# Kernel tuning notes

Hardware: AMD Instinct MI355X
Metric: run time of the kernel (lower is better)

Reference implementation:

```python
import jax, jax.numpy as jnp
import numpy as np

L = 8          # n_layer
D = 512        # hidden_size
DIN = 1024     # d_inner = 2*D (Mamba expand=2)
DS = 16        # d_state
DTR = 32       # dt_rank = ceil(D/16)
K = 4          # d_conv
NACT = 3       # n_action_to_predict
ADIM = 4
LOSS_COEF = 1.0

def silu(x):
    return x * jax.nn.sigmoid(x)

def rms(x, w, eps=1e-5):
    return x * jax.lax.rsqrt(jnp.mean(x * x, axis=-1, keepdims=True) + eps) * w

def tokenize(images, states, actions, patch_w, patch_b, state_w, state_b, act_w, act_b):
    # images [b,l,3,224,224] -> 14x14 patches of 3*16*16=768 -> mean-pooled image token
    b, l = images.shape[:2]
    p = images.reshape(b, l, 3, 14, 16, 14, 16).transpose(0, 1, 3, 5, 2, 4, 6).reshape(b, l, 196, 768)
    img = jnp.mean(p @ patch_w.T + patch_b, axis=2)            # [b,l,D] token_type 1
    st = states[:, :, 0] @ state_w.T + state_b                 # [b,l,D] token_type 2
    ac = actions[:, :, :NACT - 1] @ act_w.T + act_b            # [b,l,NACT-1,D] token_type 3
    toks = jnp.concatenate([img[:, :, None], st[:, :, None], ac], axis=2)  # [b,l,1+NACT,D]
    return toks.reshape(b, l * (1 + NACT), D)

def mamba_mixer(x, in_w, cw, cb, xpw, dtw, dtb, alog, dp, ow):
    # x: [b,S,D]
    b, S, _ = x.shape
    xz = x @ in_w.T                                   # [b,S,2*DIN]
    xi, z = xz[..., :DIN], xz[..., DIN:]
    # causal depthwise conv, kernel K
    xp = jnp.pad(xi, ((0, 0), (K - 1, 0), (0, 0)))
    xc = cb + sum(cw[:, k] * xp[:, k:k + S, :] for k in range(K))
    xc = silu(xc)
    proj = xc @ xpw.T                                  # [b,S,DTR+2*DS]
    dtr, Bm, Cm = proj[..., :DTR], proj[..., DTR:DTR + DS], proj[..., DTR + DS:]
    dt = jax.nn.softplus(dtr @ dtw.T + dtb)            # [b,S,DIN]
    A = -jnp.exp(alog)                                 # [DIN,DS]
    dA = jnp.exp(dt[..., None] * A)                    # [b,S,DIN,DS]
    dBx = dt[..., None] * Bm[:, :, None, :] * xc[..., None]
    def step(h, inp):
        a_t, bx_t = inp
        h = a_t * h + bx_t
        return h, h
    _, hs = jax.lax.scan(step, jnp.zeros((b, DIN, DS), x.dtype),
                         (dA.swapaxes(0, 1), dBx.swapaxes(0, 1)))  # hs [S,b,DIN,DS]
    y = jnp.einsum('sbdn,bsn->bsd', hs, Cm) + dp * xc
    return (y * silu(z)) @ ow.T

def _forward(images, seq_length, states, actions, action_labels,
             patch_w, patch_b, state_w, state_b, act_w, act_b,
             norm1_w, in_proj_w, conv_w, conv_b, x_proj_w, dt_w, dt_b,
             A_log, Dp, out_proj_w, norm2_w, fc1_w, fc2_w, norm_f_w,
             head_w, head_b):
    b, l = images.shape[:2]
    hidden = tokenize(images, states, actions, patch_w, patch_b, state_w, state_b, act_w, act_b)
    residual = jnp.zeros_like(hidden)
    for i in range(L):
        residual = hidden + residual
        hidden = mamba_mixer(rms(residual, norm1_w[i]), in_proj_w[i], conv_w[i], conv_b[i],
                             x_proj_w[i], dt_w[i], dt_b[i], A_log[i], Dp[i], out_proj_w[i])
        residual = hidden + residual
        g = rms(residual, norm2_w[i]) @ fc1_w[i].T       # GatedMLP fc1 -> [.., 2*DIN]
        hidden = (g[..., :DIN] * silu(g[..., DIN:])) @ fc2_w[i].T
    residual = hidden + residual
    hidden = rms(residual, norm_f_w)
    # static action-token positions: per-frame tokens [img, state, act, act] -> indices 1..3
    hs = hidden.reshape(b, l, 1 + NACT, D)[:, :, 1:, :]
    action_preds = hs @ head_w.T + head_b                # [b,l,NACT,ADIM]
    mask = (jnp.arange(l)[None, :] < seq_length[:, None]).astype(jnp.float32)
    la = jnp.mean(jnp.abs(action_preds - action_labels), axis=(2, 3))
    la = (la * mask).sum(axis=1) / jnp.clip(mask.sum(axis=1), 1.0)
    loss = jnp.mean(la) * LOSS_COEF
    return loss, action_preds

def setup_inputs() -> dict:
    key = jax.random.key(0)
    ks = iter(jax.random.split(key, 40))
    nrm = lambda shape, s=0.02: s * jax.random.normal(next(ks), shape, dtype=jnp.float32)
    inp = {
        'images': jax.random.normal(next(ks), (2, 64, 3, 224, 224), jnp.float32),
        'seq_length': jax.random.randint(next(ks), (2,), 1, 65),
        'states': jax.random.normal(next(ks), (2, 64, NACT, 7), jnp.float32),
        'actions': jax.random.normal(next(ks), (2, 64, NACT, ADIM), jnp.float32),
        'action_labels': jax.random.normal(next(ks), (2, 64, NACT, ADIM), jnp.float32),
        'patch_w': nrm((D, 768)), 'patch_b': jnp.zeros((D,), jnp.float32),
        'state_w': nrm((D, 7)), 'state_b': jnp.zeros((D,), jnp.float32),
        'act_w': nrm((D, ADIM)), 'act_b': jnp.zeros((D,), jnp.float32),
        'norm1_w': jnp.ones((L, D), jnp.float32),
        'in_proj_w': nrm((L, 2 * DIN, D)),
        'conv_w': nrm((L, DIN, K), 0.1), 'conv_b': jnp.zeros((L, DIN), jnp.float32),
        'x_proj_w': nrm((L, DTR + 2 * DS, DIN)),
        'dt_w': nrm((L, DIN, DTR)), 'dt_b': jnp.full((L, DIN), -4.6, jnp.float32),
        'A_log': jnp.log(jnp.broadcast_to(jnp.arange(1, DS + 1, dtype=jnp.float32), (L, DIN, DS))).copy(),
        'Dp': jnp.ones((L, DIN), jnp.float32),
        'out_proj_w': nrm((L, D, DIN)),
        'norm2_w': jnp.ones((L, D), jnp.float32),
        'fc1_w': nrm((L, 2 * DIN, D)), 'fc2_w': nrm((L, D, DIN)),
        'norm_f_w': jnp.ones((D,), jnp.float32),
        'head_w': nrm((ADIM, D)), 'head_b': jnp.zeros((ADIM,), jnp.float32),
    }
    return inp

def reference(images, seq_length, states, actions, action_labels,
              patch_w, patch_b, state_w, state_b, act_w, act_b,
              norm1_w, in_proj_w, conv_w, conv_b, x_proj_w, dt_w, dt_b,
              A_log, Dp, out_proj_w, norm2_w, fc1_w, fc2_w, norm_f_w,
              head_w, head_b):
    return _forward(images, seq_length, states, actions, action_labels,
                    patch_w, patch_b, state_w, state_b, act_w, act_b,
                    norm1_w, in_proj_w, conv_w, conv_b, x_proj_w, dt_w, dt_b,
                    A_log, Dp, out_proj_w, norm2_w, fc1_w, fc2_w, norm_f_w,
                    head_w, head_b)
```

## Files before the change

### kernel.cpp

```cpp
#include <hip/hip_runtime.h>


#define NTOK 512
#define SEQ  256
#define CS   32
#define NC   8

typedef __attribute__((ext_vector_type(8))) short bf16x8;
typedef __attribute__((ext_vector_type(16))) float f32x16;

__device__ __forceinline__ float silu_f(float x) { return x / (1.0f + expf(-x)); }
__device__ __forceinline__ float softplus_f(float x) {
  return (x > 20.0f) ? x : log1pf(expf(x));
}

__device__ __forceinline__ void split_pack(float4 v, uint2* hi, uint2* lo) {
  uint ux = __float_as_uint(v.x), uy = __float_as_uint(v.y);
  uint uz = __float_as_uint(v.z), uw = __float_as_uint(v.w);
  hi->x = (ux >> 16) | (uy & 0xffff0000u);
  hi->y = (uz >> 16) | (uw & 0xffff0000u);
  float lx = v.x - __uint_as_float(ux & 0xffff0000u);
  float ly = v.y - __uint_as_float(uy & 0xffff0000u);
  float lz = v.z - __uint_as_float(uz & 0xffff0000u);
  float lw = v.w - __uint_as_float(uw & 0xffff0000u);
  lo->x = (__float_as_uint(lx) >> 16) | (__float_as_uint(ly) & 0xffff0000u);
  lo->y = (__float_as_uint(lz) >> 16) | (__float_as_uint(lw) & 0xffff0000u);
}

__global__ __launch_bounds__(256) void gemm_bs_k(const float* __restrict__ A,
                                                 const float* __restrict__ B,
                                                 float* __restrict__ C,
                                                 int M, int N, int K, int Kc) {
  __shared__ alignas(16) ushort sAh[2][2][512];
  __shared__ alignas(16) ushort sAl[2][2][512];
  __shared__ alignas(16) ushort sBh[2][2][512];
  __shared__ alignas(16) ushort sBl[2][2][512];
  int t = threadIdx.x;
  int bn = blockIdx.x, bm = blockIdx.y, z = blockIdx.z;
  const float* Ab = A + (size_t)bm * 64 * K + (size_t)z * Kc;
  const float* Bb = B + (size_t)bn * 64 * K + (size_t)z * Kc;
  float* Cb = C + (size_t)z * M * N;
  int r = t >> 2, kc = (t & 3) << 2;
  int st = r >> 5, m = r & 31;
  int off = ((kc >> 3) << 8) + (m << 3) + (kc & 7);
  int w = t >> 6, lane = t & 63;
  int wr = w >> 1, wc = w & 1;

  f32x16 acc;
#pragma unroll
  for (int i = 0; i < 16; ++i) acc[i] = 0.f;

  int nk = Kc >> 4;
  float4 a4 = *(const float4*)&Ab[(size_t)r * K + kc];
  float4 b4 = *(const float4*)&Bb[(size_t)r * K + kc];
  {
    uint2 hi, lo;
    split_pack(a4, &hi, &lo);
    *(uint2*)&sAh[0][st][off] = hi; *(uint2*)&sAl[0][st][off] = lo;
    split_pack(b4, &hi, &lo);
    *(uint2*)&sBh[0][st][off] = hi; *(uint2*)&sBl[0][st][off] = lo;
  }
  __syncthreads();
  for (int ks = 0; ks < nk; ++ks) {
    int buf = ks & 1;
    if (ks + 1 < nk) {
      a4 = *(const float4*)&Ab[(size_t)r * K + (ks + 1) * 16 + kc];
      b4 = *(const float4*)&Bb[(size_t)r * K + (ks + 1) * 16 + kc];
    }
    bf16x8 ah = *(bf16x8*)&sAh[buf][wr][lane << 3];
    bf16x8 al = *(bf16x8*)&sAl[buf][wr][lane << 3];
    bf16x8 bh = *(bf16x8*)&sBh[buf][wc][lane << 3];
    bf16x8 bl = *(bf16x8*)&sBl[buf][wc][lane << 3];
    acc = __builtin_amdgcn_mfma_f32_32x32x16_bf16(ah, bh, acc, 0, 0, 0);
    acc = __builtin_amdgcn_mfma_f32_32x32x16_bf16(al, bh, acc, 0, 0, 0);
    acc = __builtin_amdgcn_mfma_f32_32x32x16_bf16(ah, bl, acc, 0, 0, 0);
    if (ks + 1 < nk) {
      uint2 hi, lo;
      split_pack(a4, &hi, &lo);
      *(uint2*)&sAh[buf ^ 1][st][off] = hi; *(uint2*)&sAl[buf ^ 1][st][off] = lo;
      split_pack(b4, &hi, &lo);
      *(uint2*)&sBh[buf ^ 1][st][off] = hi; *(uint2*)&sBl[buf ^ 1][st][off] = lo;
    }
    __syncthreads();
  }
  int col = lane & 31, rq = lane >> 5;
  float* Cw = Cb + (size_t)(bm * 64 + wr * 32) * N + bn * 64 + wc * 32 + col;
#pragma unroll
  for (int rg = 0; rg < 16; ++rg) {
    int row = (rg & 3) + ((rg >> 2) << 3) + (rq << 2);
    Cw[(size_t)row * N] = acc[rg];
  }
}

__global__ __launch_bounds__(256) void gemm_glu_k(const float* __restrict__ G,
                                                  const float* __restrict__ B,
                                                  float* __restrict__ C,
                                                  int M, int N, int K, int Kc) {
  __shared__ alignas(16) ushort sAh[2][2][512];
  __shared__ alignas(16) ushort sAl[2][2][512];
  __shared__ alignas(16) ushort sBh[2][2][512];
  __shared__ alignas(16) ushort sBl[2][2][512];
  int t = threadIdx.x;
  int bn = blockIdx.x, bm = blockIdx.y, z = blockIdx.z;
  const float* Gb = G + (size_t)bm * 64 * 2048 + (size_t)z * Kc;
  const float* Bb = B + (size_t)bn * 64 * K + (size_t)z * Kc;
  float* Cb = C + (size_t)z * M * N;
  int r = t >> 2, kc = (t & 3) << 2;
  int st = r >> 5, m = r & 31;
  int off = ((kc >> 3) << 8) + (m << 3) + (kc & 7);
  int w = t >> 6, lane = t & 63;
  int wr = w >> 1, wc = w & 1;

  f32x16 acc;
#pragma unroll
  for (int i = 0; i < 16; ++i) acc[i] = 0.f;

  int nk = Kc >> 4;
  const float* gr = Gb + (size_t)r * 2048 + kc;
  float4 ga = *(const float4*)&gr[0];
  float4 gz = *(const float4*)&gr[1024];
  float4 b4 = *(const float4*)&Bb[(size_t)r * K + kc];
  {
    float4 a4 = {ga.x * silu_f(gz.x), ga.y * silu_f(gz.y),
                 ga.z * silu_f(gz.z), ga.w * silu_f(gz.w)};
    uint2 hi, lo;
    split_pack(a4, &hi, &lo);
    *(uint2*)&sAh[0][st][off] = hi; *(uint2*)&sAl[0][st][off] = lo;
    split_pack(b4, &hi, &lo);
    *(uint2*)&sBh[0][st][off] = hi; *(uint2*)&sBl[0][st][off] = lo;
  }
  __syncthreads();
  for (int ks = 0; ks < nk; ++ks) {
    int buf = ks & 1;
    if (ks + 1 < nk) {
      ga = *(const float4*)&gr[(ks + 1) * 16];
      gz = *(const float4*)&gr[1024 + (ks + 1) * 16];
      b4 = *(const float4*)&Bb[(size_t)r * K + (ks + 1) * 16 + kc];
    }
    bf16x8 ah = *(bf16x8*)&sAh[buf][wr][lane << 3];
    bf16x8 al = *(bf16x8*)&sAl[buf][wr][lane << 3];
    bf16x8 bh = *(bf16x8*)&sBh[buf][wc][lane << 3];
    bf16x8 bl = *(bf16x8*)&sBl[buf][wc][lane << 3];
    acc = __builtin_amdgcn_mfma_f32_32x32x16_bf16(ah, bh, acc, 0, 0, 0);
    acc = __builtin_amdgcn_mfma_f32_32x32x16_bf16(al, bh, acc, 0, 0, 0);
    acc = __builtin_amdgcn_mfma_f32_32x32x16_bf16(ah, bl, acc, 0, 0, 0);
    if (ks + 1 < nk) {
      float4 a4 = {ga.x * silu_f(gz.x), ga.y * silu_f(gz.y),
                   ga.z * silu_f(gz.z), ga.w * silu_f(gz.w)};
      uint2 hi, lo;
      split_pack(a4, &hi, &lo);
      *(uint2*)&sAh[buf ^ 1][st][off] = hi; *(uint2*)&sAl[buf ^ 1][st][off] = lo;
      split_pack(b4, &hi, &lo);
      *(uint2*)&sBh[buf ^ 1][st][off] = hi; *(uint2*)&sBl[buf ^ 1][st][off] = lo;
    }
    __syncthreads();
  }
  int col = lane & 31, rq = lane >> 5;
  float* Cw = Cb + (size_t)(bm * 64 + wr * 32) * N + bn * 64 + wc * 32 + col;
#pragma unroll
  for (int rg = 0; rg < 16; ++rg) {
    int row = (rg & 3) + ((rg >> 2) << 3) + (rq << 2);
    Cw[(size_t)row * N] = acc[rg];
  }
}

__global__ void patch_part_k(const float* __restrict__ img, float* __restrict__ pmp) {
  int blk = blockIdx.x;
  int bl = blk / 14, hb = blk % 14;
  int t = threadIdx.x;
  int c = t >> 6, hi = (t >> 2) & 15, wi4 = t & 3;
  const float* base = img + (size_t)bl * 3 * 50176 + (size_t)c * 50176 +
                      (size_t)(hb * 16 + hi) * 224 + wi4 * 4;
  float4 s = {0.f, 0.f, 0.f, 0.f};
#pragma unroll
  for (int wb = 0; wb < 14; ++wb) {
    float4 v = *(const float4*)&base[wb * 16];
    s.x += v.x; s.y += v.y; s.z += v.z; s.w += v.w;
  }
  ((float4*)(pmp + (size_t)blk * 768))[t] = s;
}

__global__ void patch_red_k(const float* __restrict__ pmp, float* __restrict__ meanp) {
  int bl = blockIdx.x;
  int t = threadIdx.x;
  float4 s = {0.f, 0.f, 0.f, 0.f};
  for (int hb = 0; hb < 14; ++hb) {
    float4 v = ((const float4*)(pmp + (size_t)(bl * 14 + hb) * 768))[t];
    s.x += v.x; s.y += v.y; s.z += v.z; s.w += v.w;
  }
  const float inv = 1.0f / 196.0f;
  float4 o = {s.x * inv, s.y * inv, s.z * inv, s.w * inv};
  ((float4*)(meanp + (size_t)bl * 768))[t] = o;
}

__global__ void tokenize_k(const float* __restrict__ imgp,
                           const float* __restrict__ states,
                           const float* __restrict__ actions,
                           const float* __restrict__ pb,
                           const float* __restrict__ sw, const float* __restrict__ sb,
                           const float* __restrict__ aw, const float* __restrict__ ab,
                           float* __restrict__ hidden, float* __restrict__ residual) {
  int tok = blockIdx.x;
  int t = threadIdx.x;
  int j = tok & 3;
  int bl = tok >> 2;
  int o0 = t * 4;
  float out[4];
  if (j == 0) {
    float4 a = ((const float4*)pb)[t];
    const float* ip = imgp + (size_t)bl * 512;
#pragma unroll
    for (int p = 0; p < 8; ++p) {
      float4 v = ((const float4*)(ip + (size_t)p * 65536))[t];
      a.x += v.x; a.y += v.y; a.z += v.z; a.w += v.w;
    }
    out[0] = a.x; out[1] = a.y; out[2] = a.z; out[3] = a.w;
  } else if (j == 1) {
    const float* sv = states + (size_t)bl * 21;
#pragma unroll
    for (int i = 0; i < 4; ++i) {
      int o = o0 + i;
      float acc = sb[o];
      for (int k = 0; k < 7; ++k) acc += sw[o * 7 + k] * sv[k];
      out[i] = acc;
    }
  } else {
    const float* av = actions + ((size_t)bl * 3 + (j - 2)) * 4;
#pragma unroll
    for (int i = 0; i < 4; ++i) {
      int o = o0 + i;
      float acc = ab[o];
      for (int k = 0; k < 4; ++k) acc += aw[o * 4 + k] * av[k];
      out[i] = acc;
    }
  }
  float4 ov = {out[0], out[1], out[2], out[3]};
  ((float4*)(hidden + (size_t)tok * 512))[t] = ov;
  float4 z4 = {0.f, 0.f, 0.f, 0.f};
  ((float4*)(residual + (size_t)tok * 512))[t] = z4;
}

__global__ void addnorm_k(const float* __restrict__ hid, int parts,
                          float* __restrict__ res,
                          const float* __restrict__ w, float* __restrict__ xn) {
  int tok = blockIdx.x;
  int t = threadIdx.x;
  float4* r4 = (float4*)(res + (size_t)tok * 512);
  float4 r = r4[t];
  const float4* hp = (const float4*)(hid + (size_t)tok * 512);
  for (int p = 0; p < parts; ++p) {
    float4 h = hp[t];
    r.x += h.x; r.y += h.y; r.z += h.z; r.w += h.w;
    hp += 65536;
  }
  r4[t] = r;
  float ss = r.x * r.x + r.y * r.y + r.z * r.z + r.w * r.w;
  for (int off = 32; off; off >>= 1) ss += __shfl_down(ss, off, 64);
  __shared__ float s2[2];
  if ((t & 63) == 0) s2[t >> 6] = ss;
  __syncthreads();
  float tot = s2[0] + s2[1];
  float scale = rsqrtf(tot * (1.0f / 512.0f) + 1e-5f);
  float4 wv = ((const float4*)w)[t];
  float4 o = {r.x * scale * wv.x, r.y * scale * wv.y,
              r.z * scale * wv.z, r.w * scale * wv.w};
  ((float4*)(xn + (size_t)tok * 512))[t] = o;
}

__global__ __launch_bounds__(256) void convproj_k(const float* __restrict__ xz,
                                                  const float* __restrict__ cw,
                                                  const float* __restrict__ cb,
                                                  const float* __restrict__ xpw,
                                                  const float* __restrict__ dtw,
                                                  const float* __restrict__ dtbias,
                                                  float* __restrict__ xc,
                                                  float* __restrict__ proj,
                                                  float* __restrict__ dt) {
  int tok = blockIdx.x;
  int t = threadIdx.x;
  int b = tok >> 8, s = tok & 255;
  __shared__ float xr[1024];
  __shared__ float pp[4][64];
  __shared__ float pr[64];
  int d4 = t * 4;
  float4 cw0 = ((const float4*)cw)[d4];
  float4 cw1 = ((const float4*)cw)[d4 + 1];
  float4 cw2 = ((const float4*)cw)[d4 + 2];
  float4 cw3 = ((const float4*)cw)[d4 + 3];
  float acc0 = cb[d4], acc1 = cb[d4 + 1], acc2 = cb[d4 + 2], acc3 = cb[d4 + 3];
  const float* base = xz + (size_t)b * 256 * 2048 + d4;
  const float wk0[4] = {cw0.x, cw0.y, cw0.z, cw0.w};
  const float wk1[4] = {cw1.x, cw1.y, cw1.z, cw1.w};
  const float wk2[4] = {cw2.x, cw2.y, cw2.z, cw2.w};
  const float wk3[4] = {cw3.x, cw3.y, cw3.z, cw3.w};
#pragma unroll
  for (int k = 0; k < 4; ++k) {
    int row = s + k - 3;
    if (row >= 0) {
      float4 v = *(const float4*)&base[(size_t)row * 2048];
      acc0 += wk0[k] * v.x; acc1 += wk1[k] * v.y;
      acc2 += wk2[k] * v.z; acc3 += wk3[k] * v.w;
    }
  }
  float4 xc4 = {silu_f(acc0), silu_f(acc1), silu_f(acc2), silu_f(acc3)};
  ((float4*)(xc + (size_t)tok * 1024))[t] = xc4;
  *(float4*)&xr[d4] = xc4;
  __syncthreads();
  int n = t & 63, q = t >> 6;
  {
    const float* wrow = xpw + (size_t)n * 1024 + q * 256;
    const float* xq = xr + q * 256;
    float acc = 0.f;
    for (int k = 0; k < 256; k += 4)
      acc += wrow[k] * xq[k] + wrow[k + 1] * xq[k + 1] +
             wrow[k + 2] * xq[k + 2] + wrow[k + 3] * xq[k + 3];
    pp[q][n] = acc;
  }
  __syncthreads();
  if (t < 64) {
    float v = pp[0][t] + pp[1][t] + pp[2][t] + pp[3][t];
    pr[t] = v;
    proj[(size_t)tok * 64 + t] = v;
  }
  __syncthreads();
#pragma unroll
  for (int i = 0; i < 4; ++i) {
    int d = t * 4 + i;
    const float* dw = dtw + (size_t)d * 32;
    float a = dtbias[d];
    for (int k = 0; k < 32; ++k) a += dw[k] * pr[k];
    dt[(size_t)tok * 1024 + d] = softplus_f(a);
  }
}

__global__ __launch_bounds__(128) void scan1_k(const float* __restrict__ dt,
                                               const float* __restrict__ proj,
                                               const float* __restrict__ xc,
                                               const float* __restrict__ alog,
                                               float2* __restrict__ pairs) {
  __shared__ float sDt[CS][8];
  __shared__ float sXc[CS][8];
  __shared__ float sB[CS][16];
  int t = threadIdx.x;
  int g = blockIdx.x, c = blockIdx.y;
  int b = g >> 7;
  int d0 = (g & 127) << 3;
  int dl = t >> 4, n = t & 15;
  int d = d0 + dl;
  int s0 = c * CS;
  float A = -expf(alog[d * 16 + n]);
  const float* dtb = dt + ((size_t)b * SEQ + s0) * 1024 + d0;
  const float* xcb = xc + ((size_t)b * SEQ + s0) * 1024 + d0;
  const float* pbp = proj + ((size_t)b * SEQ + s0) * 64 + 32;
  if (t < 64) {
    int li = t >> 1, lc4 = (t & 1) * 4;
    *(float4*)&sDt[li][lc4] = *(const float4*)&dtb[(size_t)li * 1024 + lc4];
    *(float4*)&sXc[li][lc4] = *(const float4*)&xcb[(size_t)li * 1024 + lc4];
  }
  {
    int r = t >> 2, c4 = (t & 3) * 4;
    *(float4*)&sB[r][c4] = *(const float4*)&pbp[(size_t)r * 64 + c4];
  }
  __syncthreads();
  float Ap = 1.f, Bacc = 0.f;
#pragma unroll
  for (int i = 0; i < CS; ++i) {
    float dtv = sDt[i][dl];
    float dA = __expf(dtv * A);
    Bacc = dA * Bacc + dtv * sB[i][n] * sXc[i][dl];
    Ap *= dA;
  }
  pairs[(((size_t)c * 2 + b) * 1024 + d) * 16 + n] = make_float2(Ap, Bacc);
}

__global__ __launch_bounds__(128) void scan2_k(const float* __restrict__ dt,
                                               const float* __restrict__ proj,
                                               const float* __restrict__ xc,
                                               const float* __restrict__ xz,
                                               const float* __restrict__ alog,
                                               const float* __restrict__ Dp,
                                               const float2* __restrict__ pairs,
                                               float* __restrict__ yz) {
  __shared__ float sDt[CS][8];
  __shared__ float sXc[CS][8];
  __shared__ float sZ[CS][8];
  __shared__ float sBC[CS][32];
  __shared__ float sY[CS][8];
  int t = threadIdx.x;
  int g = blockIdx.x, c = blockIdx.y;
  int b = g >> 7;
  int d0 = (g & 127) << 3;
  int dl = t >> 4, n = t & 15;
  int d = d0 + dl;
  int s0 = c * CS;
  float A = -expf(alog[d * 16 + n]);
  float dp = Dp[d];
  const float* dtb = dt + ((size_t)b * SEQ + s0) * 1024 + d0;
  const float* xcb = xc + ((size_t)b * SEQ + s0) * 1024 + d0;
  const float* zb  = xz + ((size_t)b * SEQ + s0) * 2048 + 1024 + d0;
  const float* pbp = proj + ((size_t)b * SEQ + s0) * 64 + 32;
  float* yb = yz + ((size_t)b * SEQ + s0) * 1024 + d0;
  float h = 0.f;
  for (int cc = 0; cc < c; ++cc) {
    float2 p = pairs[(((size_t)cc * 2 + b) * 1024 + d) * 16 + n];
    h = p.x * h + p.y;
  }
  bool lowh = t < 64;
  int u = lowh ? t : t - 64;
  int li = u >> 1, lc4 = (u & 1) * 4;
  if (lowh) {
    *(float4*)&sDt[li][lc4] = *(const float4*)&dtb[(size_t)li * 1024 + lc4];
    *(float4*)&sXc[li][lc4] = *(const float4*)&xcb[(size_t)li * 1024 + lc4];
  } else {
    *(float4*)&sZ[li][lc4] = *(const float4*)&zb[(size_t)li * 2048 + lc4];
  }
  {
    int v0i = t >> 3, v0c = (t & 7) * 4;
    int v1i = (t + 128) >> 3, v1c = ((t + 128) & 7) * 4;
    *(float4*)&sBC[v0i][v0c] = *(const float4*)&pbp[(size_t)v0i * 64 + v0c];
    *(float4*)&sBC[v1i][v1c] = *(const float4*)&pbp[(size_t)v1i * 64 + v1c];
  }
  __syncthreads();
#pragma unroll
  for (int i = 0; i < CS; ++i) {
    float dtv = sDt[i][dl];
    float xcv = sXc[i][dl];
    float dA = __expf(dtv * A);
    h = dA * h + dtv * sBC[i][n] * xcv;
    float yc = h * sBC[i][16 + n];
    yc += __shfl_xor(yc, 1, 64);
    yc += __shfl_xor(yc, 2, 64);
    yc += __shfl_xor(yc, 4, 64);
    yc += __shfl_xor(yc, 8, 64);
    if (n == 0) sY[i][dl] = (yc + dp * xcv) * silu_f(sZ[i][dl]);
  }
  __syncthreads();
  if (lowh)
    *(float4*)&yb[(size_t)li * 1024 + lc4] = *(const float4*)&sY[li][lc4];
}

__global__ void head_k(const float* __restrict__ hf, const float* __restrict__ hw,
                       const float* __restrict__ hb, const float* __restrict__ labels,
                       float* __restrict__ preds, float* __restrict__ labs) {
  int blk = blockIdx.x;
  int j = blk % 3;
  int l = (blk / 3) % 64;
  int b = blk / 192;
  int row = b * 256 + l * 4 + 1 + j;
  int t = threadIdx.x;
  const float* x = hf + (size_t)row * 512;
  float acc[4] = {0.f, 0.f, 0.f, 0.f};
  for (int k = t; k < 512; k += 64) {
    float xv = x[k];
#pragma unroll
    for (int a = 0; a < 4; ++a) acc[a] += xv * hw[a * 512 + k];
  }
  for (int off = 32; off; off >>= 1) {
#pragma unroll
    for (int a = 0; a < 4; ++a) acc[a] += __shfl_down(acc[a], off, 64);
  }
  if (t == 0) {
    const float* lab = labels + (size_t)blk * 4;
    float sd = 0.f;
#pragma unroll
    for (int a = 0; a < 4; ++a) {
      float p = acc[a] + hb[a];
      preds[(size_t)blk * 4 + a] = p;
      sd += fabsf(p - lab[a]);
    }
    labs[blk] = sd;
  }
}

__global__ void loss_k(const float* __restrict__ labs, const int* __restrict__ seqlen,
                       float* __restrict__ out) {
  int t = threadIdx.x;
  int b = t >> 6, l = t & 63;
  float la = (labs[(b * 64 + l) * 3] + labs[(b * 64 + l) * 3 + 1] +
              labs[(b * 64 + l) * 3 + 2]) * (1.0f / 12.0f);
  float m = (l < seqlen[b]) ? 1.f : 0.f;
  float v = la * m;
  for (int off = 32; off; off >>= 1) {
    v += __shfl_down(v, off, 64);
    m += __shfl_down(m, off, 64);
  }
  __shared__ float sb_[2];
  if ((t & 63) == 0) sb_[b] = v / fmaxf(m, 1.0f);
  __syncthreads();
  if (t == 0) out[0] = 0.5f * (sb_[0] + sb_[1]);
}

extern "C" void kernel_launch(void* const* d_in, const int* in_sizes, int n_in,
                              void* d_out, int out_size, void* d_ws, size_t ws_size,
                              hipStream_t stream) {
  const float* images     = (const float*)d_in[0];
  const int*   seq_length = (const int*)d_in[1];
  const float* states     = (const float*)d_in[2];
  const float* actions    = (const float*)d_in[3];
  const float* labels     = (const float*)d_in[4];
  const float* patch_w    = (const float*)d_in[5];
  const float* patch_b    = (const float*)d_in[6];
  const float* state_w    = (const float*)d_in[7];
  const float* state_b    = (const float*)d_in[8];
  const float* act_w      = (const float*)d_in[9];
  const float* act_b      = (const float*)d_in[10];
  const float* norm1_w    = (const float*)d_in[11];
  const float* in_proj_w  = (const float*)d_in[12];
  const float* conv_w     = (const float*)d_in[13];
  const float* conv_b     = (const float*)d_in[14];
  const float* x_proj_w   = (const float*)d_in[15];
  const float* dt_w       = (const float*)d_in[16];
  const float* dt_b       = (const float*)d_in[17];
  const float* A_log      = (const float*)d_in[18];
  const float* Dp         = (const float*)d_in[19];
  const float* out_proj_w = (const float*)d_in[20];
  const float* norm2_w    = (const float*)d_in[21];
  const float* fc1_w      = (const float*)d_in[22];
  const float* fc2_w      = (const float*)d_in[23];
  const float* norm_f_w   = (const float*)d_in[24];
  const float* head_w     = (const float*)d_in[25];
  const float* head_b     = (const float*)d_in[26];

  float* out = (float*)d_out;

  float* ws = (float*)d_ws;
  float* meanp    = ws; ws += 98304;
  float* hidden   = ws; ws += 262144;
  float* residual = ws; ws += 262144;
  float* xn       = ws; ws += 262144;
  float* xz       = ws; ws += 1048576;
  float* xc       = ws; ws += 524288;
  float* proj     = ws; ws += 32768;
  float* dtbuf    = ws; ws += 524288;
  float* yz       = ws; ws += 524288;
  float* labs     = ws; ws += 384;
  float* cpart    = ws; ws += 1048576;
  float* pmp      = ws; ws += 1376256;
  float2* pairs   = (float2*)ws; ws += 524288;

  hipLaunchKernelGGL(patch_part_k, dim3(1792), dim3(192), 0, stream, images, pmp);
  hipLaunchKernelGGL(patch_red_k, dim3(128), dim3(192), 0, stream, pmp, meanp);
  hipLaunchKernelGGL(gemm_bs_k, dim3(8, 2, 8), dim3(256), 0, stream,
                     meanp, patch_w, cpart, 128, 512, 768, 96);
  hipLaunchKernelGGL(tokenize_k, dim3(512), dim3(128), 0, stream, cpart, states, actions,
                     patch_b, state_w, state_b, act_w, act_b, hidden, residual);

  for (int i = 0; i < 8; ++i) {
    const float* n1 = norm1_w + i * 512;
    const float* ipw = in_proj_w + (size_t)i * 2048 * 512;
    const float* cw = conv_w + (size_t)i * 4096;
    const float* cb = conv_b + (size_t)i * 1024;
    const float* xpw = x_proj_w + (size_t)i * 65536;
    const float* dtw = dt_w + (size_t)i * 32768;
    const float* dtbias = dt_b + (size_t)i * 1024;
    const float* al = A_log + (size_t)i * 16384;
    const float* dpp = Dp + (size_t)i * 1024;
    const float* opw = out_proj_w + (size_t)i * 524288;
    const float* n2 = norm2_w + i * 512;
    const float* f1 = fc1_w + (size_t)i * 1048576;
    const float* f2 = fc2_w + (size_t)i * 524288;

    if (i == 0)
      hipLaunchKernelGGL(addnorm_k, dim3(512), dim3(128), 0, stream,
                         hidden, 1, residual, n1, xn);
    else
      hipLaunchKernelGGL(addnorm_k, dim3(512), dim3(128), 0, stream,
                         cpart, 4, residual, n1, xn);
    hipLaunchKernelGGL(gemm_bs_k, dim3(32, 8, 1), dim3(256), 0, stream,
                       xn, ipw, xz, 512, 2048, 512, 512);
    hipLaunchKernelGGL(convproj_k, dim3(512), dim3(256), 0, stream,
                       xz, cw, cb, xpw, dtw, dtbias, xc, proj, dtbuf);
    hipLaunchKernelGGL(scan1_k, dim3(256, 8), dim3(128), 0, stream,
                       dtbuf, proj, xc, al, pairs);
    hipLaunchKernelGGL(scan2_k, dim3(256, 8), dim3(128), 0, stream,
                       dtbuf, proj, xc, xz, al, dpp, pairs, yz);
    hipLaunchKernelGGL(gemm_bs_k, dim3(8, 8, 4), dim3(256), 0, stream,
                       yz, opw, cpart, 512, 512, 1024, 256);
    hipLaunchKernelGGL(addnorm_k, dim3(512), dim3(128), 0, stream,
                       cpart, 4, residual, n2, xn);
    hipLaunchKernelGGL(gemm_bs_k, dim3(32, 8, 1), dim3(256), 0, stream,
                       xn, f1, xz, 512, 2048, 512, 512);
    hipLaunchKernelGGL(gemm_glu_k, dim3(8, 8, 4), dim3(256), 0, stream,
                       xz, f2, cpart, 512, 512, 1024, 256);
  }

  hipLaunchKernelGGL(addnorm_k, dim3(512), dim3(128), 0, stream,
                     cpart, 4, residual, norm_f_w, xn);
  hipLaunchKernelGGL(head_k, dim3(384), dim3(64), 0, stream, xn, head_w, head_b, labels,
                     out + 1, labs);
  hipLaunchKernelGGL(loss_k, dim3(1), dim3(128), 0, stream, labs, seq_length, out);
}
```

Baseline: 1.175 ms.

## Fuse residual add and RMSNorm into GEMM prologue, split K across two warp groups

Two changes. The GEMM kernels now run 512 threads: two groups of four waves each take half of every 32-wide K step, and their partial sums are combined through shared memory before the store. Separately, a new gemm_an_k kernel does the residual add and RMSNorm in the prologue of the in_proj and fc1 GEMMs. This removes the standalone addnorm launches and the xn round trip, and residual ping-pongs between two buffers. The cost is that every column block recomputes the row norm and reads the residual and partial rows again, and register pressure rises from holding 16 float4 per thread.

```diff
diff --git a/kernel.cpp b/kernel.cpp
--- a/kernel.cpp
+++ b/kernel.cpp
@@ -27,95 +27,108 @@
   lo->y = (__float_as_uint(lz) >> 16) | (__float_as_uint(lw) & 0xffff0000u);
 }
 
-__global__ __launch_bounds__(256) void gemm_bs_k(const float* __restrict__ A,
+__global__ __launch_bounds__(512) void gemm_bs_k(const float* __restrict__ A,
                                                  const float* __restrict__ B,
                                                  float* __restrict__ C,
                                                  int M, int N, int K, int Kc) {
-  __shared__ alignas(16) ushort sAh[2][2][512];
-  __shared__ alignas(16) ushort sAl[2][2][512];
-  __shared__ alignas(16) ushort sBh[2][2][512];
-  __shared__ alignas(16) ushort sBl[2][2][512];
+  __shared__ alignas(16) ushort sAh[2][2][2][512];
+  __shared__ alignas(16) ushort sAl[2][2][2][512];
+  __shared__ alignas(16) ushort sBh[2][2][2][512];
+  __shared__ alignas(16) ushort sBl[2][2][2][512];
+  __shared__ alignas(64) float sRed[4096];
   int t = threadIdx.x;
   int bn = blockIdx.x, bm = blockIdx.y, z = blockIdx.z;
   const float* Ab = A + (size_t)bm * 64 * K + (size_t)z * Kc;
   const float* Bb = B + (size_t)bn * 64 * K + (size_t)z * Kc;
   float* Cb = C + (size_t)z * M * N;
-  int r = t >> 2, kc = (t & 3) << 2;
+  int r = t >> 3, kc = (t & 7) << 2;
+  int kh = kc >> 4, kc16 = kc & 15;
   int st = r >> 5, m = r & 31;
-  int off = ((kc >> 3) << 8) + (m << 3) + (kc & 7);
+  int off = ((kc16 >> 3) << 8) + (m << 3) + (kc16 & 7);
   int w = t >> 6, lane = t & 63;
-  int wr = w >> 1, wc = w & 1;
+  int g = w >> 2, wq = w & 3;
+  int wr = wq >> 1, wc = wq & 1;
 
   f32x16 acc;
 #pragma unroll
   for (int i = 0; i < 16; ++i) acc[i] = 0.f;
 
-  int nk = Kc >> 4;
+  int ns = Kc >> 5;
   float4 a4 = *(const float4*)&Ab[(size_t)r * K + kc];
   float4 b4 = *(const float4*)&Bb[(size_t)r * K + kc];
   {
     uint2 hi, lo;
     split_pack(a4, &hi, &lo);
-    *(uint2*)&sAh[0][st][off] = hi; *(uint2*)&sAl[0][st][off] = lo;
+    *(uint2*)&sAh[0][kh][st][off] = hi; *(uint2*)&sAl[0][kh][st][off] = lo;
     split_pack(b4, &hi, &lo);
-    *(uint2*)&sBh[0][st][off] = hi; *(uint2*)&sBl[0][st][off] = lo;
-  }
-  __syncthreads();
-  for (int ks = 0; ks < nk; ++ks) {
-    int buf = ks & 1;
-    if (ks + 1 < nk) {
-      a4 = *(const float4*)&Ab[(size_t)r * K + (ks + 1) * 16 + kc];
-      b4 = *(const float4*)&Bb[(size_t)r * K + (ks + 1) * 16 + kc];
-    }
-    bf16x8 ah = *(bf16x8*)&sAh[buf][wr][lane << 3];
-    bf16x8 al = *(bf16x8*)&sAl[buf][wr][lane << 3];
-    bf16x8 bh = *(bf16x8*)&sBh[buf][wc][lane << 3];
-    bf16x8 bl = *(bf16x8*)&sBl[buf][wc][lane << 3];
+    *(uint2*)&sBh[0][kh][st][off] = hi; *(uint2*)&sBl[0][kh][st][off] = lo;
+  }
+  __syncthreads();
+  for (int ssi = 0; ssi < ns; ++ssi) {
+    int buf = ssi & 1;
+    if (ssi + 1 < ns) {
+      a4 = *(const float4*)&Ab[(size_t)r * K + (ssi + 1) * 32 + kc];
+      b4 = *(const float4*)&Bb[(size_t)r * K + (ssi + 1) * 32 + kc];
+    }
+    bf16x8 ah = *(bf16x8*)&sAh[buf][g][wr][lane << 3];
+    bf16x8 al = *(bf16x8*)&sAl[buf][g][wr][lane << 3];
+    bf16x8 bh = *(bf16x8*)&sBh[buf][g][wc][lane << 3];
+    bf16x8 bl = *(bf16x8*)&sBl[buf][g][wc][lane << 3];
     acc = __builtin_amdgcn_mfma_f32_32x32x16_bf16(ah, bh, acc, 0, 0, 0);
     acc = __builtin_amdgcn_mfma_f32_32x32x16_bf16(al, bh, acc, 0, 0, 0);
     acc = __builtin_amdgcn_mfma_f32_32x32x16_bf16(ah, bl, acc, 0, 0, 0);
-    if (ks + 1 < nk) {
+    if (ssi + 1 < ns) {
       uint2 hi, lo;
       split_pack(a4, &hi, &lo);
-      *(uint2*)&sAh[buf ^ 1][st][off] = hi; *(uint2*)&sAl[buf ^ 1][st][off] = lo;
+      *(uint2*)&sAh[buf ^ 1][kh][st][off] = hi; *(uint2*)&sAl[buf ^ 1][kh][st][off] = lo;
       split_pack(b4, &hi, &lo);
-      *(uint2*)&sBh[buf ^ 1][st][off] = hi; *(uint2*)&sBl[buf ^ 1][st][off] = lo;
+      *(uint2*)&sBh[buf ^ 1][kh][st][off] = hi; *(uint2*)&sBl[buf ^ 1][kh][st][off] = lo;
     }
     __syncthreads();
   }
-  int col = lane & 31, rq = lane >> 5;
-  float* Cw = Cb + (size_t)(bm * 64 + wr * 32) * N + bn * 64 + wc * 32 + col;
-#pragma unroll
-  for (int rg = 0; rg < 16; ++rg) {
-    int row = (rg & 3) + ((rg >> 2) << 3) + (rq << 2);
-    Cw[(size_t)row * N] = acc[rg];
-  }
-}
-
-__global__ __launch_bounds__(256) void gemm_glu_k(const float* __restrict__ G,
+  if (g == 1) *(f32x16*)&sRed[(wq * 64 + lane) << 4] = acc;
+  __syncthreads();
+  if (g == 0) {
+    f32x16 o = *(f32x16*)&sRed[(wq * 64 + lane) << 4];
+#pragma unroll
+    for (int i = 0; i < 16; ++i) acc[i] += o[i];
+    int col = lane & 31, rq = lane >> 5;
+    float* Cw = Cb + (size_t)(bm * 64 + wr * 32) * N + bn * 64 + wc * 32 + col;
+#pragma unroll
+    for (int rg = 0; rg < 16; ++rg) {
+      int row = (rg & 3) + ((rg >> 2) << 3) + (rq << 2);
+      Cw[(size_t)row * N] = acc[rg];
+    }
+  }
+}
+
+__global__ __launch_bounds__(512) void gemm_glu_k(const float* __restrict__ G,
                                                   const float* __restrict__ B,
                                                   float* __restrict__ C,
                                                   int M, int N, int K, int Kc) {
-  __shared__ alignas(16) ushort sAh[2][2][512];
-  __shared__ alignas(16) ushort sAl[2][2][512];
-  __shared__ alignas(16) ushort sBh[2][2][512];
-  __shared__ alignas(16) ushort sBl[2][2][512];
+  __shared__ alignas(16) ushort sAh[2][2][2][512];
+  __shared__ alignas(16) ushort sAl[2][2][2][512];
+  __shared__ alignas(16) ushort sBh[2][2][2][512];
+  __shared__ alignas(16) ushort sBl[2][2][2][512];
+  __shared__ alignas(64) float sRed[4096];
   int t = threadIdx.x;
   int bn = blockIdx.x, bm = blockIdx.y, z = blockIdx.z;
   const float* Gb = G + (size_t)bm * 64 * 2048 + (size_t)z * Kc;
   const float* Bb = B + (size_t)bn * 64 * K + (size_t)z * Kc;
   float* Cb = C + (size_t)z * M * N;
-  int r = t >> 2, kc = (t & 3) << 2;
+  int r = t >> 3, kc = (t & 7) << 2;
+  int kh = kc >> 4, kc16 = kc & 15;
   int st = r >> 5, m = r & 31;
-  int off = ((kc >> 3) << 8) + (m << 3) + (kc & 7);
+  int off = ((kc16 >> 3) << 8) + (m << 3) + (kc16 & 7);
   int w = t >> 6, lane = t & 63;
-  int wr = w >> 1, wc = w & 1;
+  int g = w >> 2, wq = w & 3;
+  int wr = wq >> 1, wc = wq & 1;
 
   f32x16 acc;
 #pragma unroll
   for (int i = 0; i < 16; ++i) acc[i] = 0.f;
 
-  int nk = Kc >> 4;
+  int ns = Kc >> 5;
   const float* gr = Gb + (size_t)r * 2048 + kc;
   float4 ga = *(const float4*)&gr[0];
   float4 gz = *(const float4*)&gr[1024];
@@ -125,42 +138,155 @@
                  ga.z * silu_f(gz.z), ga.w * silu_f(gz.w)};
     uint2 hi, lo;
     split_pack(a4, &hi, &lo);
-    *(uint2*)&sAh[0][st][off] = hi; *(uint2*)&sAl[0][st][off] = lo;
+    *(uint2*)&sAh[0][kh][st][off] = hi; *(uint2*)&sAl[0][kh][st][off] = lo;
     split_pack(b4, &hi, &lo);
-    *(uint2*)&sBh[0][st][off] = hi; *(uint2*)&sBl[0][st][off] = lo;
-  }
-  __syncthreads();
-  for (int ks = 0; ks < nk; ++ks) {
-    int buf = ks & 1;
-    if (ks + 1 < nk) {
-      ga = *(const float4*)&gr[(ks + 1) * 16];
-      gz = *(const float4*)&gr[1024 + (ks + 1) * 16];
-      b4 = *(const float4*)&Bb[(size_t)r * K + (ks + 1) * 16 + kc];
-    }
-    bf16x8 ah = *(bf16x8*)&sAh[buf][wr][lane << 3];
-    bf16x8 al = *(bf16x8*)&sAl[buf][wr][lane << 3];
-    bf16x8 bh = *(bf16x8*)&sBh[buf][wc][lane << 3];
-    bf16x8 bl = *(bf16x8*)&sBl[buf][wc][lane << 3];
+    *(uint2*)&sBh[0][kh][st][off] = hi; *(uint2*)&sBl[0][kh][st][off] = lo;
+  }
+  __syncthreads();
+  for (int ssi = 0; ssi < ns; ++ssi) {
+    int buf = ssi & 1;
+    if (ssi + 1 < ns) {
+      ga = *(const float4*)&gr[(ssi + 1) * 32];
+      gz = *(const float4*)&gr[1024 + (ssi + 1) * 32];
+      b4 = *(const float4*)&Bb[(size_t)r * K + (ssi + 1) * 32 + kc];
+    }
+    bf16x8 ah = *(bf16x8*)&sAh[buf][g][wr][lane << 3];
+    bf16x8 al = *(bf16x8*)&sAl[buf][g][wr][lane << 3];
+    bf16x8 bh = *(bf16x8*)&sBh[buf][g][wc][lane << 3];
+    bf16x8 bl = *(bf16x8*)&sBl[buf][g][wc][lane << 3];
     acc = __builtin_amdgcn_mfma_f32_32x32x16_bf16(ah, bh, acc, 0, 0, 0);
     acc = __builtin_amdgcn_mfma_f32_32x32x16_bf16(al, bh, acc, 0, 0, 0);
     acc = __builtin_amdgcn_mfma_f32_32x32x16_bf16(ah, bl, acc, 0, 0, 0);
-    if (ks + 1 < nk) {
+    if (ssi + 1 < ns) {
       float4 a4 = {ga.x * silu_f(gz.x), ga.y * silu_f(gz.y),
                    ga.z * silu_f(gz.z), ga.w * silu_f(gz.w)};
       uint2 hi, lo;
       split_pack(a4, &hi, &lo);
-      *(uint2*)&sAh[buf ^ 1][st][off] = hi; *(uint2*)&sAl[buf ^ 1][st][off] = lo;
+      *(uint2*)&sAh[buf ^ 1][kh][st][off] = hi; *(uint2*)&sAl[buf ^ 1][kh][st][off] = lo;
       split_pack(b4, &hi, &lo);
-      *(uint2*)&sBh[buf ^ 1][st][off] = hi; *(uint2*)&sBl[buf ^ 1][st][off] = lo;
+      *(uint2*)&sBh[buf ^ 1][kh][st][off] = hi; *(uint2*)&sBl[buf ^ 1][kh][st][off] = lo;
     }
     __syncthreads();
   }
-  int col = lane & 31, rq = lane >> 5;
-  float* Cw = Cb + (size_t)(bm * 64 + wr * 32) * N + bn * 64 + wc * 32 + col;
-#pragma unroll
-  for (int rg = 0; rg < 16; ++rg) {
-    int row = (rg & 3) + ((rg >> 2) << 3) + (rq << 2);
-    Cw[(size_t)row * N] = acc[rg];
+  if (g == 1) *(f32x16*)&sRed[(wq * 64 + lane) << 4] = acc;
+  __syncthreads();
+  if (g == 0) {
+    f32x16 o = *(f32x16*)&sRed[(wq * 64 + lane) << 4];
+#pragma unroll
+    for (int i = 0; i < 16; ++i) acc[i] += o[i];
+    int col = lane & 31, rq = lane >> 5;
+    float* Cw = Cb + (size_t)(bm * 64 + wr * 32) * N + bn * 64 + wc * 32 + col;
+#pragma unroll
+    for (int rg = 0; rg < 16; ++rg) {
+      int row = (rg & 3) + ((rg >> 2) << 3) + (rq << 2);
+      Cw[(size_t)row * N] = acc[rg];
+    }
+  }
+}
+
+__global__ __launch_bounds__(512) void gemm_an_k(const float* __restrict__ Hid,
+                                                 int parts,
+                                                 const float* __restrict__ res_in,
+                                                 float* __restrict__ res_out,
+                                                 const float* __restrict__ nw,
+                                                 const float* __restrict__ B,
+                                                 float* __restrict__ C, int N) {
+  __shared__ alignas(16) ushort sAh[2][2][2][512];
+  __shared__ alignas(16) ushort sAl[2][2][2][512];
+  __shared__ alignas(16) ushort sBh[2][2][2][512];
+  __shared__ alignas(16) ushort sBl[2][2][2][512];
+  __shared__ alignas(64) float sRed[4096];
+  int t = threadIdx.x;
+  int bn = blockIdx.x, bm = blockIdx.y;
+  const float* Bb = B + (size_t)bn * 64 * 512;
+  int r = t >> 3, kc = (t & 7) << 2;
+  int row = bm * 64 + r;
+  int kh = kc >> 4, kc16 = kc & 15;
+  int st = r >> 5, m = r & 31;
+  int off = ((kc16 >> 3) << 8) + (m << 3) + (kc16 & 7);
+  int w = t >> 6, lane = t & 63;
+  int g = w >> 2, wq = w & 3;
+  int wr = wq >> 1, wc = wq & 1;
+
+  float4 rv[16];
+  float ss = 0.f;
+  {
+    const float* rp = res_in + (size_t)row * 512 + kc;
+    const float* hp = Hid + (size_t)row * 512 + kc;
+#pragma unroll
+    for (int j = 0; j < 16; ++j) {
+      float4 v = *(const float4*)&rp[j * 32];
+      for (int p = 0; p < parts; ++p) {
+        float4 h = *(const float4*)&hp[(size_t)p * 262144 + j * 32];
+        v.x += h.x; v.y += h.y; v.z += h.z; v.w += h.w;
+      }
+      rv[j] = v;
+      ss += v.x * v.x + v.y * v.y + v.z * v.z + v.w * v.w;
+    }
+  }
+  if (bn == 0) {
+    float* ro = res_out + (size_t)row * 512 + kc;
+#pragma unroll
+    for (int j = 0; j < 16; ++j) *(float4*)&ro[j * 32] = rv[j];
+  }
+  ss += __shfl_xor(ss, 1, 64);
+  ss += __shfl_xor(ss, 2, 64);
+  ss += __shfl_xor(ss, 4, 64);
+  float scale = rsqrtf(ss * (1.0f / 512.0f) + 1e-5f);
+#pragma unroll
+  for (int j = 0; j < 16; ++j) {
+    float4 wv = *(const float4*)&nw[kc + j * 32];
+    rv[j].x *= scale * wv.x; rv[j].y *= scale * wv.y;
+    rv[j].z *= scale * wv.z; rv[j].w *= scale * wv.w;
+  }
+
+  f32x16 acc;
+#pragma unroll
+  for (int i = 0; i < 16; ++i) acc[i] = 0.f;
+
+  float4 b4 = *(const float4*)&Bb[(size_t)r * 512 + kc];
+  {
+    uint2 hi, lo;
+    split_pack(rv[0], &hi, &lo);
+    *(uint2*)&sAh[0][kh][st][off] = hi; *(uint2*)&sAl[0][kh][st][off] = lo;
+    split_pack(b4, &hi, &lo);
+    *(uint2*)&sBh[0][kh][st][off] = hi; *(uint2*)&sBl[0][kh][st][off] = lo;
+  }
+  __syncthreads();
+#pragma unroll
+  for (int ssi = 0; ssi < 16; ++ssi) {
+    int buf = ssi & 1;
+    if (ssi + 1 < 16)
+      b4 = *(const float4*)&Bb[(size_t)r * 512 + (ssi + 1) * 32 + kc];
+    bf16x8 ah = *(bf16x8*)&sAh[buf][g][wr][lane << 3];
+    bf16x8 al = *(bf16x8*)&sAl[buf][g][wr][lane << 3];
+    bf16x8 bh = *(bf16x8*)&sBh[buf][g][wc][lane << 3];
+    bf16x8 bl = *(bf16x8*)&sBl[buf][g][wc][lane << 3];
+    acc = __builtin_amdgcn_mfma_f32_32x32x16_bf16(ah, bh, acc, 0, 0, 0);
+    acc = __builtin_amdgcn_mfma_f32_32x32x16_bf16(al, bh, acc, 0, 0, 0);
+    acc = __builtin_amdgcn_mfma_f32_32x32x16_bf16(ah, bl, acc, 0, 0, 0);
+    if (ssi + 1 < 16) {
+      uint2 hi, lo;
+      split_pack(rv[ssi + 1], &hi, &lo);
+      *(uint2*)&sAh[buf ^ 1][kh][st][off] = hi; *(uint2*)&sAl[buf ^ 1][kh][st][off] = lo;
+      split_pack(b4, &hi, &lo);
+      *(uint2*)&sBh[buf ^ 1][kh][st][off] = hi; *(uint2*)&sBl[buf ^ 1][kh][st][off] = lo;
+    }
+    __syncthreads();
+  }
+  if (g == 1) *(f32x16*)&sRed[(wq * 64 + lane) << 4] = acc;
+  __syncthreads();
+  if (g == 0) {
+    f32x16 o = *(f32x16*)&sRed[(wq * 64 + lane) << 4];
+#pragma unroll
+    for (int i = 0; i < 16; ++i) acc[i] += o[i];
+    int col = lane & 31, rq = lane >> 5;
+    float* Cw = C + (size_t)(bm * 64 + wr * 32) * N + bn * 64 + wc * 32 + col;
+#pragma unroll
+    for (int rg = 0; rg < 16; ++rg) {
+      int row2 = (rg & 3) + ((rg >> 2) << 3) + (rq << 2);
+      Cw[(size_t)row2 * N] = acc[rg];
+    }
   }
 }
 
@@ -527,6 +653,7 @@
   float* meanp    = ws; ws += 98304;
   float* hidden   = ws; ws += 262144;
   float* residual = ws; ws += 262144;
+  float* residual2= ws; ws += 262144;
   float* xn       = ws; ws += 262144;
   float* xz       = ws; ws += 1048576;
   float* xc       = ws; ws += 524288;
@@ -540,7 +667,7 @@
 
   hipLaunchKernelGGL(patch_part_k, dim3(1792), dim3(192), 0, stream, images, pmp);
   hipLaunchKernelGGL(patch_red_k, dim3(128), dim3(192), 0, stream, pmp, meanp);
-  hipLaunchKernelGGL(gemm_bs_k, dim3(8, 2, 8), dim3(256), 0, stream,
+  hipLaunchKernelGGL(gemm_bs_k, dim3(8, 2, 8), dim3(512), 0, stream,
                      meanp, patch_w, cpart, 128, 512, 768, 96);
   hipLaunchKernelGGL(tokenize_k, dim3(512), dim3(128), 0, stream, cpart, states, actions,
                      patch_b, state_w, state_b, act_w, act_b, hidden, residual);
@@ -560,27 +687,21 @@
     const float* f1 = fc1_w + (size_t)i * 1048576;
     const float* f2 = fc2_w + (size_t)i * 524288;
 
-    if (i == 0)
-      hipLaunchKernelGGL(addnorm_k, dim3(512), dim3(128), 0, stream,
-                         hidden, 1, residual, n1, xn);
-    else
-      hipLaunchKernelGGL(addnorm_k, dim3(512), dim3(128), 0, stream,
-                         cpart, 4, residual, n1, xn);
-    hipLaunchKernelGGL(gemm_bs_k, dim3(32, 8, 1), dim3(256), 0, stream,
-                       xn, ipw, xz, 512, 2048, 512, 512);
+    const float* hid_in = (i == 0) ? hidden : cpart;
+    int parts = (i == 0) ? 1 : 4;
+    hipLaunchKernelGGL(gemm_an_k, dim3(32, 8), dim3(512), 0, stream,
+                       hid_in, parts, residual, residual2, n1, ipw, xz, 2048);
     hipLaunchKernelGGL(convproj_k, dim3(512), dim3(256), 0, stream,
                        xz, cw, cb, xpw, dtw, dtbias, xc, proj, dtbuf);
     hipLaunchKernelGGL(scan1_k, dim3(256, 8), dim3(128), 0, stream,
                        dtbuf, proj, xc, al, pairs);
     hipLaunchKernelGGL(scan2_k, dim3(256, 8), dim3(128), 0, stream,
                        dtbuf, proj, xc, xz, al, dpp, pairs, yz);
-    hipLaunchKernelGGL(gemm_bs_k, dim3(8, 8, 4), dim3(256), 0, stream,
+    hipLaunchKernelGGL(gemm_bs_k, dim3(8, 8, 4), dim3(512), 0, stream,
                        yz, opw, cpart, 512, 512, 1024, 256);
-    hipLaunchKernelGGL(addnorm_k, dim3(512), dim3(128), 0, stream,
-                       cpart, 4, residual, n2, xn);
-    hipLaunchKernelGGL(gemm_bs_k, dim3(32, 8, 1), dim3(256), 0, stream,
-                       xn, f1, xz, 512, 2048, 512, 512);
-    hipLaunchKernelGGL(gemm_glu_k, dim3(8, 8, 4), dim3(256), 0, stream,
+    hipLaunchKernelGGL(gemm_an_k, dim3(32, 8), dim3(512), 0, stream,
+                       cpart, 4, residual2, residual, n2, f1, xz, 2048);
+    hipLaunchKernelGGL(gemm_glu_k, dim3(8, 8, 4), dim3(512), 0, stream,
                        xz, f2, cpart, 512, 512, 1024, 256);
   }
 
```

Measured after the change: 1.361 ms. 1.16x slower.
